# Optimization experiments

Measured on AMD Instinct MI355X. Metric: run time of the kernel, lower is better.

Reference implementation:

```python
import jax, jax.numpy as jnp
import numpy as np

N_FEATURES = 16
NUM_LAYERS = 8
HIDDEN = 256
NUM_BINS = 8
RANGE_MIN, RANGE_MAX = -5.0, 5.0
MIN_BIN = 1e-4      # distrax RationalQuadraticSpline min_bin_size
MIN_SLOPE = 1e-4    # distrax min_knot_slope
LOC_ALPHA = 1.0
BATCH = 131072


def setup_inputs() -> dict:
    key = jax.random.key(0)
    ks = jax.random.split(key, 8)
    L, F, H = NUM_LAYERS, N_FEATURES, HIDDEN
    P = F * (3 * NUM_BINS + 1)  # 400
    x = jax.random.normal(ks[0], (BATCH, F), dtype=jnp.float32)
    # first Dense: variance_scaling(0.01,'fan_in','normal')
    W0 = (jax.random.normal(ks[1], (L, F, H)) * np.sqrt(0.01 / F)).astype(jnp.float32)
    b0 = jnp.zeros((L, H), jnp.float32)
    # residual-block denses (lecun-normal scale)
    Wr = (jax.random.normal(ks[2], (L, 4, H, H)) / np.sqrt(H)).astype(jnp.float32)
    br = jnp.zeros((L, 4, H), jnp.float32)
    # final Dense is zero-init in the module; use small random values so the
    # spline branch actually computes non-identity math for kernel testing.
    Wf = (jax.random.normal(ks[3], (L, H, P)) * 0.01).astype(jnp.float32)
    bf = (jax.random.normal(ks[4], (L, P)) * 0.01).astype(jnp.float32)
    scales = (1.0 + 0.05 * jax.random.normal(ks[5], (L, F))).astype(jnp.float32)
    shifts = (0.05 * jax.random.normal(ks[6], (L, F))).astype(jnp.float32)
    rng = np.random.RandomState(0)
    perms = jnp.array(np.stack([rng.permutation(F) for _ in range(L)]).astype(np.int32))
    return dict(x=x, W0=W0, b0=b0, Wr=Wr, br=br, Wf=Wf, bf=bf,
                scales=scales, shifts=shifts, perms=perms)


def _pe_mask(dtype):
    # sin_pe_func(pe_op='add', pe_t=1.0, pe_alpha=loc_alpha, pe_ratio=1.0)
    idx = jnp.arange(HIDDEN, dtype=dtype) / HIDDEN
    return LOC_ALPHA * jnp.sin(2.0 * jnp.pi * idx)


def _conditioner(xm, W0, b0, Wr, br, Wf, bf, pe):
    h = xm @ W0 + b0                                  # (B,H)
    for blk in range(2):
        y = h
        for j in range(2):
            y = jax.nn.relu(y + pe) @ Wr[2 * blk + j] + br[2 * blk + j]
        h = h + y
    h = jax.nn.relu(h)
    p = h @ Wf + bf                                   # (B, F*25)
    return p.reshape(p.shape[0], N_FEATURES, 3 * NUM_BINS + 1)


def _rqs_forward(x, params):
    # distrax RationalQuadraticSpline.forward_and_log_det, vectorized over (B,F)
    K = NUM_BINS
    uw, uh, us = params[..., :K], params[..., K:2 * K], params[..., 2 * K:]
    total = RANGE_MAX - RANGE_MIN
    w = jax.nn.softmax(uw, axis=-1) * (total - K * MIN_BIN) + MIN_BIN
    h = jax.nn.softmax(uh, axis=-1) * (total - K * MIN_BIN) + MIN_BIN
    offset = float(np.log(np.expm1(1.0 - MIN_SLOPE)))
    d = jax.nn.softplus(us + offset) + MIN_SLOPE       # (B,F,K+1) knot slopes
    zeros = jnp.zeros(x.shape + (1,), x.dtype)
    xk = RANGE_MIN + jnp.concatenate([zeros, jnp.cumsum(w, -1)], -1)  # (B,F,K+1)
    yk = RANGE_MIN + jnp.concatenate([zeros, jnp.cumsum(h, -1)], -1)
    idx = jnp.clip(jnp.sum((x[..., None] >= xk).astype(jnp.int32), -1) - 1, 0, K - 1)
    g = lambda a, i: jnp.take_along_axis(a, i[..., None], axis=-1)[..., 0]
    x0, x1 = g(xk, idx), g(xk, idx + 1)
    y0, y1 = g(yk, idx), g(yk, idx + 1)
    d0, d1 = g(d, idx), g(d, idx + 1)
    s = (y1 - y0) / (x1 - x0)
    z = jnp.clip((x - x0) / (x1 - x0), 0.0, 1.0)
    z1m = 1.0 - z
    den = s + (d1 + d0 - 2.0 * s) * z * z1m
    y_in = y0 + (y1 - y0) * (s * z * z + d0 * z * z1m) / den
    ld_in = (2.0 * jnp.log(s)
             + jnp.log(d1 * z * z + 2.0 * s * z * z1m + d0 * z1m * z1m)
             - 2.0 * jnp.log(den))
    inside = (x >= RANGE_MIN) & (x <= RANGE_MAX)      # identity outside range
    return jnp.where(inside, y_in, x), jnp.where(inside, ld_in, 0.0)


def _flow_log_prob(x, W0, b0, Wr, br, Wf, bf, scales, shifts, perms):
    B, F = x.shape
    pe = _pe_mask(x.dtype)
    mask = (jnp.arange(F) % 2).astype(bool)  # True = pass-through dim
    logdet = jnp.zeros((B,), x.dtype)
    for i in range(NUM_LAYERS):
        x = x[:, perms[i]]                                   # Permute (logdet 0)
        x = x * scales[i] + shifts[i]                        # all-dims ScalarAffine
        logdet = logdet + jnp.sum(jnp.log(jnp.abs(scales[i])))
        xm = jnp.where(mask, x, jnp.zeros_like(x))           # conditioner sees masked x
        params = _conditioner(xm, W0[i], b0[i], Wr[i], br[i], Wf[i], bf[i], pe)
        y, ld = _rqs_forward(x, params)                      # masked RQS coupling
        x = jnp.where(mask, x, y)
        logdet = logdet + jnp.sum(jnp.where(mask, jnp.zeros_like(ld), ld), axis=-1)
        mask = ~mask
    base_lp = -0.5 * jnp.sum(x * x, axis=-1) - 0.5 * F * jnp.log(2.0 * jnp.pi)
    return base_lp + logdet


def reference(x, W0, b0, Wr, br, Wf, bf, scales, shifts, perms):
    return _flow_log_prob(x, W0, b0, Wr, br, Wf, bf, scales, shifts, perms)
```

## Files before the change

kernel.cpp:

```cpp
#include <hip/hip_runtime.h>

#define NBATCH   131072
#define FDIM     16
#define NLAYER   8
#define HDIM     256
#define PCOLS    208
#define PSTRIDE  212
#define TSTRIDE  264
#define MTILE    64
#define NTHREADS 256
#define TBUF     (MTILE*TSTRIDE)

typedef unsigned short u16;
typedef __attribute__((ext_vector_type(8))) __bf16 bf16x8;
typedef __attribute__((ext_vector_type(8))) u16    u16x8;
typedef __attribute__((ext_vector_type(4))) u16    u16x4;
typedef __attribute__((ext_vector_type(2))) u16    u16x2;
typedef __attribute__((ext_vector_type(4))) float  f32x4;

#define WRP_OFF  0u
#define W0P_OFF  4194304u
#define WFP_OFF  4325376u
#define BFP_OFF  5177344u

__device__ __forceinline__ u16 f2bf(float f){
  __bf16 h = (__bf16)f;
  return __builtin_bit_cast(u16, h);
}
__device__ __forceinline__ float bf2f(u16 b){
  unsigned u = ((unsigned)b) << 16;
  return __builtin_bit_cast(float, u);
}
__device__ __forceinline__ f32x4 mfma16(bf16x8 a, bf16x8 b, f32x4 c){
  return __builtin_amdgcn_mfma_f32_16x16x32_bf16(a, b, c, 0, 0, 0);
}

__global__ void pack_wr_k(const float* __restrict__ Wr, u16* __restrict__ Wrp){
  int idx = blockIdx.x*256 + threadIdx.x;
  int n = idx & 255, g = (idx>>8)&3, ks = (idx>>10)&7, m = (idx>>13)&3, l = idx>>15;
  const float* src = Wr + (((size_t)(l*4+m)*HDIM + (ks*32+g*8))*HDIM + n);
  u16x8 v;
  #pragma unroll
  for (int j=0;j<8;++j) v[j] = f2bf(src[(size_t)j*HDIM]);
  *(u16x8*)(Wrp + (size_t)idx*8) = v;
}
__global__ void pack_w0_k(const float* __restrict__ W0, u16* __restrict__ W0p){
  int idx = blockIdx.x*256 + threadIdx.x;
  int n = idx&255, g=(idx>>8)&3, l=idx>>10;
  u16x8 v;
  #pragma unroll
  for (int j=0;j<8;++j){ int k=g*8+j; v[j] = (k<FDIM) ? f2bf(W0[(l*FDIM+k)*HDIM+n]) : (u16)0; }
  *(u16x8*)(W0p + (size_t)idx*8) = v;
}
__global__ void pack_wf_k(const float* __restrict__ Wf, u16* __restrict__ Wfp){
  int idx = blockIdx.x*256 + threadIdx.x;
  int nc = idx % PCOLS; int t = idx / PCOLS;
  int g = t&3, ks=(t>>2)&7, l=t>>5;
  int fs = nc/26, kk = nc%26;
  u16x8 v = {0,0,0,0,0,0,0,0};
  if (kk < 25){
    int f = 2*fs + (l&1);
    int col = f*25 + kk;
    #pragma unroll
    for (int j=0;j<8;++j){ int k=ks*32+g*8+j; v[j]=f2bf(Wf[((size_t)l*HDIM+k)*400+col]); }
  }
  *(u16x8*)(Wfp + (size_t)idx*8) = v;
}
__global__ void pack_bf_k(const float* __restrict__ bf, const float* __restrict__ scales,
                          float* __restrict__ bfp){
  int idx = blockIdx.x*256 + threadIdx.x;
  if (idx >= NLAYER*PCOLS) return;
  if (idx == NLAYER*PCOLS-1){
    float s = 0.f;
    for (int i=0;i<NLAYER*FDIM;++i) s += __logf(fabsf(scales[i]));
    bfp[idx] = s;
    return;
  }
  int nc = idx % PCOLS, l = idx / PCOLS;
  int fs = nc/26, kk = nc%26;
  float v = 0.f;
  if (kk < 25){ int f=2*fs+(l&1); v = bf[l*400 + f*25 + kk]; }
  bfp[idx] = v;
}

__global__ __launch_bounds__(NTHREADS, 2)
void flow_kernel(const float* __restrict__ xg,
                 const float* __restrict__ b0g,
                 const float* __restrict__ brg,
                 const float* __restrict__ scg,
                 const float* __restrict__ shg,
                 const int*   __restrict__ pmg,
                 const u16*   __restrict__ w0p,
                 const u16*   __restrict__ wrp,
                 const u16*   __restrict__ wfp,
                 const float* __restrict__ bfp,
                 float* __restrict__ outg)
{
  __shared__ u16   t_lds[2*TBUF];
  __shared__ float x_lds[MTILE*FDIM];
  __shared__ float pe_lds[HDIM];

  const int tid  = threadIdx.x;
  const int wn   = tid >> 6;
  const int lane = tid & 63;
  const int lr = lane & 15;
  const int lg = lane >> 4;
  const int rowg0 = blockIdx.x * MTILE;
  const int srow = tid >> 2;
  const int sq   = tid & 3;

  if (tid < HDIM) pe_lds[tid] = sinf(6.283185307179586f * (float)tid / 256.0f);

  {
    float4 v = *(const float4*)(xg + (size_t)(rowg0+srow)*FDIM + sq*4);
    *(float4*)(x_lds + srow*FDIM + sq*4) = v;
  }
  float ld_acc = 0.f;
  __syncthreads();

  const bf16x8* wrp8 = (const bf16x8*)wrp;
  const bf16x8* w0p8 = (const bf16x8*)w0p;
  const bf16x8* wfp8 = (const bf16x8*)wfp;

  f32x4 h[16];

  auto stage_frags = [&](u16* tbase, const f32x4* src, bool use_pe){
    #pragma unroll
    for (int mi=0; mi<4; ++mi){
      u16* dst = tbase + (mi*16 + lr)*TSTRIDE;
      #pragma unroll
      for (int ni=0; ni<4; ++ni){
        const int col = wn*64 + ni*16 + lg*4;
        f32x4 v = src[mi*4+ni];
        if (use_pe){
          f32x4 pv = *(const f32x4*)(pe_lds + col);
          #pragma unroll
          for (int r=0;r<4;++r) v[r] += pv[r];
        }
        u16x4 pk;
        #pragma unroll
        for (int r=0;r<4;++r) pk[r] = f2bf(fmaxf(v[r], 0.f));
        *(u16x4*)(dst + col) = pk;
      }
    }
  };

  auto mm_hidden = [&](const u16* tbase, f32x4* acc, const bf16x8* wb8,
                       const float* brp, bool accum){
    f32x4 res[16];
    #pragma unroll
    for (int ni=0; ni<4; ++ni){
      f32x4 bv = *(const f32x4*)(brp + wn*64 + ni*16 + lg*4);
      #pragma unroll
      for (int mi=0; mi<4; ++mi){
        f32x4 r0;
        #pragma unroll
        for (int r=0;r<4;++r) r0[r] = (accum ? acc[mi*4+ni][r] : 0.f) + bv[r];
        res[mi*4+ni] = r0;
      }
    }
    const int bofs  = lg*256 + wn*64 + lr;
    const int abase = lr*TSTRIDE;
    #pragma unroll
    for (int ks=0; ks<8; ++ks){
      bf16x8 w[4], a[4];
      #pragma unroll
      for (int ni=0; ni<4; ++ni)
        w[ni] = wb8[ks*1024 + bofs + ni*16];
      #pragma unroll
      for (int mi=0; mi<4; ++mi)
        a[mi] = *(const bf16x8*)(tbase + abase + mi*16*TSTRIDE + ks*32 + lg*8);
      #pragma unroll
      for (int mi=0; mi<4; ++mi)
        #pragma unroll
        for (int ni=0; ni<4; ++ni)
          res[mi*4+ni] = mfma16(w[ni], a[mi], res[mi*4+ni]);
    }
    #pragma unroll
    for (int i=0;i<16;++i) acc[i] = res[i];
  };

  int tb = 0;

  for (int li=0; li<NLAYER; ++li){
    u16* buf0 = t_lds + tb*TBUF;
    u16* buf1 = t_lds + (tb^1)*TBUF;

    {
      float tv[4];
      #pragma unroll
      for (int j=0;j<4;++j){
        const int f  = sq*4 + j;
        const int pf = pmg[li*FDIM + f];
        const float sc = scg[li*FDIM + f];
        tv[j] = x_lds[srow*FDIM + pf]*sc + shg[li*FDIM + f];
      }
      #pragma unroll
      for (int j=0;j<4;++j) x_lds[srow*FDIM + sq*4 + j] = tv[j];
    }

    {
      u16x8 pk;
      #pragma unroll
      for (int j=0;j<8;++j){
        const int f = sq*8 + j;
        float v = 0.f;
        if (f < FDIM && ((f & 1) != (li & 1))) v = x_lds[srow*FDIM + f];
        pk[j] = f2bf(v);
      }
      *(u16x8*)(buf0 + srow*TSTRIDE + sq*8) = pk;
    }
    __syncthreads();

    {
      bf16x8 w[4];
      #pragma unroll
      for (int ni=0; ni<4; ++ni)
        w[ni] = w0p8[li*1024 + lg*256 + wn*64 + ni*16 + lr];
      #pragma unroll
      for (int mi=0; mi<4; ++mi){
        bf16x8 a = *(const bf16x8*)(buf0 + (mi*16 + lr)*TSTRIDE + lg*8);
        #pragma unroll
        for (int ni=0; ni<4; ++ni){
          f32x4 z = {0.f,0.f,0.f,0.f};
          h[mi*4+ni] = mfma16(w[ni], a, z);
        }
      }
      #pragma unroll
      for (int ni=0; ni<4; ++ni){
        f32x4 bv = *(const f32x4*)(b0g + li*HDIM + wn*64 + ni*16 + lg*4);
        #pragma unroll
        for (int mi=0; mi<4; ++mi){
          #pragma unroll
          for (int r=0;r<4;++r) h[mi*4+ni][r] += bv[r];
        }
      }
    }

    f32x4 y[16];
    stage_frags(buf1, h, true);
    __syncthreads();
    mm_hidden(buf1, y, wrp8 + (size_t)(li*4 + 0)*8192, brg + (li*4 + 0)*HDIM, false);
    stage_frags(buf0, y, true);
    __syncthreads();
    mm_hidden(buf0, h, wrp8 + (size_t)(li*4 + 1)*8192, brg + (li*4 + 1)*HDIM, true);
    stage_frags(buf1, h, true);
    __syncthreads();
    mm_hidden(buf1, y, wrp8 + (size_t)(li*4 + 2)*8192, brg + (li*4 + 2)*HDIM, false);
    stage_frags(buf0, y, true);
    __syncthreads();
    mm_hidden(buf0, h, wrp8 + (size_t)(li*4 + 3)*8192, brg + (li*4 + 3)*HDIM, true);

    stage_frags(buf1, h, false);
    __syncthreads();
    {
      const int NFRAG = (wn==0) ? 4 : 3;
      f32x4 pacc[16];
      #pragma unroll
      for (int i=0;i<16;++i){ f32x4 z={0.f,0.f,0.f,0.f}; pacc[i]=z; }
      const int abase = lr*TSTRIDE;
      #pragma unroll
      for (int ks=0; ks<8; ++ks){
        bf16x8 a[4];
        #pragma unroll
        for (int mi=0;mi<4;++mi)
          a[mi] = *(const bf16x8*)(buf1 + abase + mi*16*TSTRIDE + ks*32 + lg*8);
        #pragma unroll
        for (int t=0;t<4;++t){
          if (t < NFRAG){
            const int nf = wn + 4*t;
            bf16x8 w = wfp8[li*6656 + ks*832 + lg*208 + nf*16 + lr];
            #pragma unroll
            for (int mi=0;mi<4;++mi)
              pacc[mi*4+t] = mfma16(w, a[mi], pacc[mi*4+t]);
          }
        }
      }
      #pragma unroll
      for (int t=0;t<4;++t){
        if (t < NFRAG){
          const int nf = wn + 4*t;
          const int col = nf*16 + lg*4;
          f32x4 bv = *(const f32x4*)(bfp + li*PCOLS + col);
          #pragma unroll
          for (int mi=0;mi<4;++mi){
            const int prow = mi*16 + lr;
            u16x4 pk;
            #pragma unroll
            for (int r=0;r<4;++r) pk[r] = f2bf(pacc[mi*4+t][r] + bv[r]);
            *(u16x4*)(buf0 + prow*PSTRIDE + col) = pk;
          }
        }
      }
    }
    __syncthreads();

    {
      #pragma unroll
      for (int e=0; e<2; ++e){
        const int fslot = sq*2 + e;
        const int ft = fslot*2 + (li & 1);
        const float xv = x_lds[srow*FDIM + ft];
        const u16* pp = buf0 + srow*PSTRIDE + fslot*26;
        float uw[8], uh[8], us[9];
        #pragma unroll
        for (int k2=0;k2<4;++k2){ u16x2 v = *(const u16x2*)(pp + 2*k2);      uw[2*k2]=bf2f(v[0]); uw[2*k2+1]=bf2f(v[1]); }
        #pragma unroll
        for (int k2=0;k2<4;++k2){ u16x2 v = *(const u16x2*)(pp + 8 + 2*k2);  uh[2*k2]=bf2f(v[0]); uh[2*k2+1]=bf2f(v[1]); }
        #pragma unroll
        for (int k2=0;k2<4;++k2){ u16x2 v = *(const u16x2*)(pp + 16 + 2*k2); us[2*k2]=bf2f(v[0]); us[2*k2+1]=bf2f(v[1]); }
        us[8] = bf2f(pp[24]);
        float mw = uw[0], mh = uh[0];
        #pragma unroll
        for (int k=1;k<8;++k){ mw=fmaxf(mw,uw[k]); mh=fmaxf(mh,uh[k]); }
        float sw=0.f, sh=0.f, bw[8], bh[8];
        #pragma unroll
        for (int k=0;k<8;++k){ bw[k]=__expf(uw[k]-mw); sw+=bw[k]; bh[k]=__expf(uh[k]-mh); sh+=bh[k]; }
        const float wscl = 9.9992f / sw;
        const float hscl = 9.9992f / sh;
        #pragma unroll
        for (int k=0;k<8;++k){ bw[k]=bw[k]*wscl + 1e-4f; bh[k]=bh[k]*hscl + 1e-4f; }
        float dv[9];
        #pragma unroll
        for (int k=0;k<9;++k){
          const float v = us[k] + 0.5411667f;
          const float spv = (v > 15.f) ? v : __logf(1.f + __expf(v));
          dv[k] = spv + 1e-4f;
        }
        const float xr = xv + 5.f;
        float cw=0.f, ch=0.f;
        float x0=0.f, y0=0.f, x1=0.f, y1=0.f, d0=0.f, d1=0.f;
        #pragma unroll
        for (int k=0;k<8;++k){
          const float nw = cw + bw[k];
          const float nh = ch + bh[k];
          const bool take = (k==0) || (xr >= cw);
          if (take){ x0=cw; y0=ch; x1=nw; y1=nh; d0=dv[k]; d1=dv[k+1]; }
          cw = nw; ch = nh;
        }
        const float dx = x1 - x0;
        const float s  = (y1 - y0) / dx;
        float z = (xr - x0) / dx;
        z = fminf(fmaxf(z, 0.f), 1.f);
        const float zm  = 1.f - z;
        const float den = s + (d1 + d0 - 2.f*s)*z*zm;
        const float yout = (y0 - 5.f) + (y1 - y0)*(s*z*z + d0*z*zm)/den;
        const float nrm  = d1*z*z + 2.f*s*z*zm + d0*zm*zm;
        const float ld   = __logf(s*s*nrm/(den*den));
        const bool inside = (xv >= -5.f) && (xv <= 5.f);
        x_lds[srow*FDIM + ft] = inside ? yout : xv;
        ld_acc += inside ? ld : 0.f;
      }
    }
    tb ^= 1;
  }

  {
    float s2 = 0.f;
    #pragma unroll
    for (int j=0;j<4;++j){
      const float xv = x_lds[srow*FDIM + sq*4 + j];
      s2 += xv*xv;
    }
    float tot = ld_acc - 0.5f*s2;
    tot += __shfl_xor(tot, 1);
    tot += __shfl_xor(tot, 2);
    if (sq == 0){
      const float sumlogsc = bfp[NLAYER*PCOLS - 1];
      outg[rowg0 + srow] = tot + sumlogsc - 14.70301653127476f;
    }
  }
}

extern "C" void kernel_launch(void* const* d_in, const int* in_sizes, int n_in,
                              void* d_out, int out_size, void* d_ws, size_t ws_size,
                              hipStream_t stream) {
  (void)in_sizes; (void)n_in; (void)out_size; (void)ws_size;
  const float* x  = (const float*)d_in[0];
  const float* W0 = (const float*)d_in[1];
  const float* b0 = (const float*)d_in[2];
  const float* Wr = (const float*)d_in[3];
  const float* br = (const float*)d_in[4];
  const float* Wf = (const float*)d_in[5];
  const float* bf = (const float*)d_in[6];
  const float* sc = (const float*)d_in[7];
  const float* sh = (const float*)d_in[8];
  const int*   pm = (const int*)d_in[9];

  char* ws = (char*)d_ws;
  u16*   Wrp = (u16*)(ws + WRP_OFF);
  u16*   W0p = (u16*)(ws + W0P_OFF);
  u16*   Wfp = (u16*)(ws + WFP_OFF);
  float* bfp = (float*)(ws + BFP_OFF);

  pack_wr_k<<<1024, 256, 0, stream>>>(Wr, Wrp);
  pack_w0_k<<<32,   256, 0, stream>>>(W0, W0p);
  pack_wf_k<<<208,  256, 0, stream>>>(Wf, Wfp);
  pack_bf_k<<<7,    256, 0, stream>>>(bf, sc, bfp);

  flow_kernel<<<NBATCH/MTILE, NTHREADS, 0, stream>>>(
      x, b0, br, sc, sh, pm, W0p, Wrp, Wfp, bfp, (float*)d_out);
}
```

Before: 1.006 ms.

## Double block to 512 threads, each wave covering half the hidden columns

```diff
diff --git a/kernel.cpp b/kernel.cpp
--- a/kernel.cpp
+++ b/kernel.cpp
@@ -8,7 +8,7 @@
 #define PSTRIDE  212
 #define TSTRIDE  264
 #define MTILE    64
-#define NTHREADS 256
+#define NTHREADS 512
 #define TBUF     (MTILE*TSTRIDE)
 
 typedef unsigned short u16;
@@ -83,7 +83,7 @@
   bfp[idx] = v;
 }
 
-__global__ __launch_bounds__(NTHREADS, 2)
+__global__ __launch_bounds__(NTHREADS, 3)
 void flow_kernel(const float* __restrict__ xg,
                  const float* __restrict__ b0g,
                  const float* __restrict__ brg,
@@ -106,14 +106,15 @@
   const int lr = lane & 15;
   const int lg = lane >> 4;
   const int rowg0 = blockIdx.x * MTILE;
-  const int srow = tid >> 2;
-  const int sq   = tid & 3;
+  const int srow = tid >> 3;
+  const int sq8  = tid & 7;
 
   if (tid < HDIM) pe_lds[tid] = sinf(6.283185307179586f * (float)tid / 256.0f);
 
-  {
-    float4 v = *(const float4*)(xg + (size_t)(rowg0+srow)*FDIM + sq*4);
-    *(float4*)(x_lds + srow*FDIM + sq*4) = v;
+  if (tid < 256){
+    const int r4 = tid >> 2, q4 = tid & 3;
+    float4 v = *(const float4*)(xg + (size_t)(rowg0+r4)*FDIM + q4*4);
+    *(float4*)(x_lds + r4*FDIM + q4*4) = v;
   }
   float ld_acc = 0.f;
   __syncthreads();
@@ -122,16 +123,16 @@
   const bf16x8* w0p8 = (const bf16x8*)w0p;
   const bf16x8* wfp8 = (const bf16x8*)wfp;
 
-  f32x4 h[16];
+  f32x4 h[8];
 
   auto stage_frags = [&](u16* tbase, const f32x4* src, bool use_pe){
     #pragma unroll
     for (int mi=0; mi<4; ++mi){
       u16* dst = tbase + (mi*16 + lr)*TSTRIDE;
       #pragma unroll
-      for (int ni=0; ni<4; ++ni){
-        const int col = wn*64 + ni*16 + lg*4;
-        f32x4 v = src[mi*4+ni];
+      for (int ni=0; ni<2; ++ni){
+        const int col = wn*32 + ni*16 + lg*4;
+        f32x4 v = src[mi*2+ni];
         if (use_pe){
           f32x4 pv = *(const f32x4*)(pe_lds + col);
           #pragma unroll
@@ -147,25 +148,25 @@
 
   auto mm_hidden = [&](const u16* tbase, f32x4* acc, const bf16x8* wb8,
                        const float* brp, bool accum){
-    f32x4 res[16];
-    #pragma unroll
-    for (int ni=0; ni<4; ++ni){
-      f32x4 bv = *(const f32x4*)(brp + wn*64 + ni*16 + lg*4);
+    f32x4 res[8];
+    #pragma unroll
+    for (int ni=0; ni<2; ++ni){
+      f32x4 bv = *(const f32x4*)(brp + wn*32 + ni*16 + lg*4);
       #pragma unroll
       for (int mi=0; mi<4; ++mi){
         f32x4 r0;
         #pragma unroll
-        for (int r=0;r<4;++r) r0[r] = (accum ? acc[mi*4+ni][r] : 0.f) + bv[r];
-        res[mi*4+ni] = r0;
-      }
-    }
-    const int bofs  = lg*256 + wn*64 + lr;
+        for (int r=0;r<4;++r) r0[r] = (accum ? acc[mi*2+ni][r] : 0.f) + bv[r];
+        res[mi*2+ni] = r0;
+      }
+    }
+    const int bofs  = lg*256 + wn*32 + lr;
     const int abase = lr*TSTRIDE;
     #pragma unroll
     for (int ks=0; ks<8; ++ks){
-      bf16x8 w[4], a[4];
-      #pragma unroll
-      for (int ni=0; ni<4; ++ni)
+      bf16x8 w[2], a[4];
+      #pragma unroll
+      for (int ni=0; ni<2; ++ni)
         w[ni] = wb8[ks*1024 + bofs + ni*16];
       #pragma unroll
       for (int mi=0; mi<4; ++mi)
@@ -173,11 +174,11 @@
       #pragma unroll
       for (int mi=0; mi<4; ++mi)
         #pragma unroll
-        for (int ni=0; ni<4; ++ni)
-          res[mi*4+ni] = mfma16(w[ni], a[mi], res[mi*4+ni]);
-    }
-    #pragma unroll
-    for (int i=0;i<16;++i) acc[i] = res[i];
+        for (int ni=0; ni<2; ++ni)
+          res[mi*2+ni] = mfma16(w[ni], a[mi], res[mi*2+ni]);
+    }
+    #pragma unroll
+    for (int i=0;i<8;++i) acc[i] = res[i];
   };
 
   int tb = 0;
@@ -187,57 +188,57 @@
     u16* buf1 = t_lds + (tb^1)*TBUF;
 
     {
-      float tv[4];
-      #pragma unroll
-      for (int j=0;j<4;++j){
-        const int f  = sq*4 + j;
+      float tv[2];
+      #pragma unroll
+      for (int j=0;j<2;++j){
+        const int f  = sq8*2 + j;
         const int pf = pmg[li*FDIM + f];
         const float sc = scg[li*FDIM + f];
         tv[j] = x_lds[srow*FDIM + pf]*sc + shg[li*FDIM + f];
       }
       #pragma unroll
-      for (int j=0;j<4;++j) x_lds[srow*FDIM + sq*4 + j] = tv[j];
+      for (int j=0;j<2;++j) x_lds[srow*FDIM + sq8*2 + j] = tv[j];
     }
 
     {
-      u16x8 pk;
-      #pragma unroll
-      for (int j=0;j<8;++j){
-        const int f = sq*8 + j;
+      u16x4 pk;
+      #pragma unroll
+      for (int j=0;j<4;++j){
+        const int f = sq8*4 + j;
         float v = 0.f;
         if (f < FDIM && ((f & 1) != (li & 1))) v = x_lds[srow*FDIM + f];
         pk[j] = f2bf(v);
       }
-      *(u16x8*)(buf0 + srow*TSTRIDE + sq*8) = pk;
+      *(u16x4*)(buf0 + srow*TSTRIDE + sq8*4) = pk;
     }
     __syncthreads();
 
     {
-      bf16x8 w[4];
-      #pragma unroll
-      for (int ni=0; ni<4; ++ni)
-        w[ni] = w0p8[li*1024 + lg*256 + wn*64 + ni*16 + lr];
+      bf16x8 w[2];
+      #pragma unroll
+      for (int ni=0; ni<2; ++ni)
+        w[ni] = w0p8[li*1024 + lg*256 + wn*32 + ni*16 + lr];
       #pragma unroll
       for (int mi=0; mi<4; ++mi){
         bf16x8 a = *(const bf16x8*)(buf0 + (mi*16 + lr)*TSTRIDE + lg*8);
         #pragma unroll
-        for (int ni=0; ni<4; ++ni){
+        for (int ni=0; ni<2; ++ni){
           f32x4 z = {0.f,0.f,0.f,0.f};
-          h[mi*4+ni] = mfma16(w[ni], a, z);
+          h[mi*2+ni] = mfma16(w[ni], a, z);
         }
       }
       #pragma unroll
-      for (int ni=0; ni<4; ++ni){
-        f32x4 bv = *(const f32x4*)(b0g + li*HDIM + wn*64 + ni*16 + lg*4);
+      for (int ni=0; ni<2; ++ni){
+        f32x4 bv = *(const f32x4*)(b0g + li*HDIM + wn*32 + ni*16 + lg*4);
         #pragma unroll
         for (int mi=0; mi<4; ++mi){
           #pragma unroll
-          for (int r=0;r<4;++r) h[mi*4+ni][r] += bv[r];
+          for (int r=0;r<4;++r) h[mi*2+ni][r] += bv[r];
         }
       }
     }
 
-    f32x4 y[16];
+    f32x4 y[8];
     stage_frags(buf1, h, true);
     __syncthreads();
     mm_hidden(buf1, y, wrp8 + (size_t)(li*4 + 0)*8192, brg + (li*4 + 0)*HDIM, false);
@@ -254,10 +255,10 @@
     stage_frags(buf1, h, false);
     __syncthreads();
     {
-      const int NFRAG = (wn==0) ? 4 : 3;
-      f32x4 pacc[16];
-      #pragma unroll
-      for (int i=0;i<16;++i){ f32x4 z={0.f,0.f,0.f,0.f}; pacc[i]=z; }
+      const int NFRAG = (wn < 5) ? 2 : 1;
+      f32x4 pacc[8];
+      #pragma unroll
+      for (int i=0;i<8;++i){ f32x4 z={0.f,0.f,0.f,0.f}; pacc[i]=z; }
       const int abase = lr*TSTRIDE;
       #pragma unroll
       for (int ks=0; ks<8; ++ks){
@@ -266,20 +267,20 @@
         for (int mi=0;mi<4;++mi)
           a[mi] = *(const bf16x8*)(buf1 + abase + mi*16*TSTRIDE + ks*32 + lg*8);
         #pragma unroll
-        for (int t=0;t<4;++t){
+        for (int t=0;t<2;++t){
           if (t < NFRAG){
-            const int nf = wn + 4*t;
+            const int nf = wn + 8*t;
             bf16x8 w = wfp8[li*6656 + ks*832 + lg*208 + nf*16 + lr];
             #pragma unroll
             for (int mi=0;mi<4;++mi)
-              pacc[mi*4+t] = mfma16(w, a[mi], pacc[mi*4+t]);
+              pacc[mi*2+t] = mfma16(w, a[mi], pacc[mi*2+t]);
           }
         }
       }
       #pragma unroll
-      for (int t=0;t<4;++t){
+      for (int t=0;t<2;++t){
         if (t < NFRAG){
-          const int nf = wn + 4*t;
+          const int nf = wn + 8*t;
           const int col = nf*16 + lg*4;
           f32x4 bv = *(const f32x4*)(bfp + li*PCOLS + col);
           #pragma unroll
@@ -287,7 +288,7 @@
             const int prow = mi*16 + lr;
             u16x4 pk;
             #pragma unroll
-            for (int r=0;r<4;++r) pk[r] = f2bf(pacc[mi*4+t][r] + bv[r]);
+            for (int r=0;r<4;++r) pk[r] = f2bf(pacc[mi*2+t][r] + bv[r]);
             *(u16x4*)(buf0 + prow*PSTRIDE + col) = pk;
           }
         }
@@ -296,61 +297,58 @@
     __syncthreads();
 
     {
-      #pragma unroll
-      for (int e=0; e<2; ++e){
-        const int fslot = sq*2 + e;
-        const int ft = fslot*2 + (li & 1);
-        const float xv = x_lds[srow*FDIM + ft];
-        const u16* pp = buf0 + srow*PSTRIDE + fslot*26;
-        float uw[8], uh[8], us[9];
-        #pragma unroll
-        for (int k2=0;k2<4;++k2){ u16x2 v = *(const u16x2*)(pp + 2*k2);      uw[2*k2]=bf2f(v[0]); uw[2*k2+1]=bf2f(v[1]); }
-        #pragma unroll
-        for (int k2=0;k2<4;++k2){ u16x2 v = *(const u16x2*)(pp + 8 + 2*k2);  uh[2*k2]=bf2f(v[0]); uh[2*k2+1]=bf2f(v[1]); }
-        #pragma unroll
-        for (int k2=0;k2<4;++k2){ u16x2 v = *(const u16x2*)(pp + 16 + 2*k2); us[2*k2]=bf2f(v[0]); us[2*k2+1]=bf2f(v[1]); }
-        us[8] = bf2f(pp[24]);
-        float mw = uw[0], mh = uh[0];
-        #pragma unroll
-        for (int k=1;k<8;++k){ mw=fmaxf(mw,uw[k]); mh=fmaxf(mh,uh[k]); }
-        float sw=0.f, sh=0.f, bw[8], bh[8];
-        #pragma unroll
-        for (int k=0;k<8;++k){ bw[k]=__expf(uw[k]-mw); sw+=bw[k]; bh[k]=__expf(uh[k]-mh); sh+=bh[k]; }
-        const float wscl = 9.9992f / sw;
-        const float hscl = 9.9992f / sh;
-        #pragma unroll
-        for (int k=0;k<8;++k){ bw[k]=bw[k]*wscl + 1e-4f; bh[k]=bh[k]*hscl + 1e-4f; }
-        float dv[9];
-        #pragma unroll
-        for (int k=0;k<9;++k){
-          const float v = us[k] + 0.5411667f;
-          const float spv = (v > 15.f) ? v : __logf(1.f + __expf(v));
-          dv[k] = spv + 1e-4f;
-        }
-        const float xr = xv + 5.f;
-        float cw=0.f, ch=0.f;
-        float x0=0.f, y0=0.f, x1=0.f, y1=0.f, d0=0.f, d1=0.f;
-        #pragma unroll
-        for (int k=0;k<8;++k){
-          const float nw = cw + bw[k];
-          const float nh = ch + bh[k];
-          const bool take = (k==0) || (xr >= cw);
-          if (take){ x0=cw; y0=ch; x1=nw; y1=nh; d0=dv[k]; d1=dv[k+1]; }
-          cw = nw; ch = nh;
-        }
-        const float dx = x1 - x0;
-        const float s  = (y1 - y0) / dx;
-        float z = (xr - x0) / dx;
-        z = fminf(fmaxf(z, 0.f), 1.f);
-        const float zm  = 1.f - z;
-        const float den = s + (d1 + d0 - 2.f*s)*z*zm;
-        const float yout = (y0 - 5.f) + (y1 - y0)*(s*z*z + d0*z*zm)/den;
-        const float nrm  = d1*z*z + 2.f*s*z*zm + d0*zm*zm;
-        const float ld   = __logf(s*s*nrm/(den*den));
-        const bool inside = (xv >= -5.f) && (xv <= 5.f);
-        x_lds[srow*FDIM + ft] = inside ? yout : xv;
-        ld_acc += inside ? ld : 0.f;
-      }
+      const int fslot = sq8;
+      const int ft = fslot*2 + (li & 1);
+      const float xv = x_lds[srow*FDIM + ft];
+      const u16* pp = buf0 + srow*PSTRIDE + fslot*26;
+      float uw[8], uh[8], us[9];
+      #pragma unroll
+      for (int k2=0;k2<4;++k2){ u16x2 v = *(const u16x2*)(pp + 2*k2);      uw[2*k2]=bf2f(v[0]); uw[2*k2+1]=bf2f(v[1]); }
+      #pragma unroll
+      for (int k2=0;k2<4;++k2){ u16x2 v = *(const u16x2*)(pp + 8 + 2*k2);  uh[2*k2]=bf2f(v[0]); uh[2*k2+1]=bf2f(v[1]); }
+      #pragma unroll
+      for (int k2=0;k2<4;++k2){ u16x2 v = *(const u16x2*)(pp + 16 + 2*k2); us[2*k2]=bf2f(v[0]); us[2*k2+1]=bf2f(v[1]); }
+      us[8] = bf2f(pp[24]);
+      float mw = uw[0], mh = uh[0];
+      #pragma unroll
+      for (int k=1;k<8;++k){ mw=fmaxf(mw,uw[k]); mh=fmaxf(mh,uh[k]); }
+      float sw=0.f, sh=0.f, bw[8], bh[8];
+      #pragma unroll
+      for (int k=0;k<8;++k){ bw[k]=__expf(uw[k]-mw); sw+=bw[k]; bh[k]=__expf(uh[k]-mh); sh+=bh[k]; }
+      const float wscl = 9.9992f / sw;
+      const float hscl = 9.9992f / sh;
+      #pragma unroll
+      for (int k=0;k<8;++k){ bw[k]=bw[k]*wscl + 1e-4f; bh[k]=bh[k]*hscl + 1e-4f; }
+      float dv[9];
+      #pragma unroll
+      for (int k=0;k<9;++k){
+        const float v = us[k] + 0.5411667f;
+        const float spv = (v > 15.f) ? v : __logf(1.f + __expf(v));
+        dv[k] = spv + 1e-4f;
+      }
+      const float xr = xv + 5.f;
+      float cw=0.f, ch=0.f;
+      float x0=0.f, y0=0.f, x1=0.f, y1=0.f, d0=0.f, d1=0.f;
+      #pragma unroll
+      for (int k=0;k<8;++k){
+        const float nw = cw + bw[k];
+        const float nh = ch + bh[k];
+        const bool take = (k==0) || (xr >= cw);
+        if (take){ x0=cw; y0=ch; x1=nw; y1=nh; d0=dv[k]; d1=dv[k+1]; }
+        cw = nw; ch = nh;
+      }
+      const float dx = x1 - x0;
+      const float s  = (y1 - y0) / dx;
+      float z = (xr - x0) / dx;
+      z = fminf(fmaxf(z, 0.f), 1.f);
+      const float zm  = 1.f - z;
+      const float den = s + (d1 + d0 - 2.f*s)*z*zm;
+      const float yout = (y0 - 5.f) + (y1 - y0)*(s*z*z + d0*z*zm)/den;
+      const float nrm  = d1*z*z + 2.f*s*z*zm + d0*zm*zm;
+      const float ld   = __logf(s*s*nrm/(den*den));
+      const bool inside = (xv >= -5.f) && (xv <= 5.f);
+      x_lds[srow*FDIM + ft] = inside ? yout : xv;
+      ld_acc += inside ? ld : 0.f;
     }
     tb ^= 1;
   }
@@ -358,14 +356,15 @@
   {
     float s2 = 0.f;
     #pragma unroll
-    for (int j=0;j<4;++j){
-      const float xv = x_lds[srow*FDIM + sq*4 + j];
+    for (int j=0;j<2;++j){
+      const float xv = x_lds[srow*FDIM + sq8*2 + j];
       s2 += xv*xv;
     }
     float tot = ld_acc - 0.5f*s2;
     tot += __shfl_xor(tot, 1);
     tot += __shfl_xor(tot, 2);
-    if (sq == 0){
+    tot += __shfl_xor(tot, 4);
+    if (sq8 == 0){
       const float sumlogsc = bfp[NLAYER*PCOLS - 1];
       outg[rowg0 + srow] = tot + sumlogsc - 14.70301653127476f;
     }
```

Result: slower. 1.489 ms (+47.9%).
